# Kernel tuning notes

Hardware: AMD Instinct MI355X
Metric: run time of the kernel (lower is better)

## Reference

```python
import jax, jax.numpy as jnp
import numpy as np

CURV_BOUNDS = (-2.0, 2.0)
THRESH = 0.01   # |k| below this -> Euclidean branch
EPS = 1e-5

B, S, D = 4, 2048, 512


def setup_inputs() -> dict:
    key = jax.random.key(0)
    ks = jax.random.split(key, 8)
    x = jax.random.normal(ks[0], (B, S, D), jnp.float32)
    sc = 1.0 / np.sqrt(D)  # ~ nn.Linear default init scale
    Wq = jax.random.uniform(ks[1], (D, D), jnp.float32, -sc, sc)
    bq = jax.random.uniform(ks[2], (D,), jnp.float32, -sc, sc)
    Wk = jax.random.uniform(ks[3], (D, D), jnp.float32, -sc, sc)
    bk = jax.random.uniform(ks[4], (D,), jnp.float32, -sc, sc)
    Wv = jax.random.uniform(ks[5], (D, D), jnp.float32, -sc, sc)
    bv = jax.random.uniform(ks[6], (D,), jnp.float32, -sc, sc)
    curvature_raw = jnp.float32(0.5)   # init_curvature
    temperature = jnp.float32(1.0)
    mask = jnp.triu(jnp.ones((S, S), dtype=bool), 1)  # causal: True = masked out
    return {"x": x, "Wq": Wq, "bq": bq, "Wk": Wk, "bk": bk, "Wv": Wv,
            "bv": bv, "curvature_raw": curvature_raw,
            "temperature": temperature, "mask": mask}


def _curvature(raw):
    k_min, k_max = CURV_BOUNDS
    return k_min + (k_max - k_min) * (jnp.tanh(raw) + 1.0) / 2.0


def _project(u, k):
    # project_to_manifold: identity (euclid), Poincare-ball clip (k<0), sphere renorm (k>0)
    n = jnp.sqrt(jnp.sum(u * u, axis=-1, keepdims=True) + 1e-12)
    absk = jnp.abs(k)
    sk = jnp.sqrt(jnp.maximum(absk, EPS))
    max_norm = (1.0 - 1e-3) / sk                      # ball radius 1/sqrt(|k|)
    u_hyp = u * jnp.minimum(1.0, max_norm / n)
    u_sph = u / (n * sk)                              # sphere radius 1/sqrt(k)
    return jnp.where(absk < THRESH, u, jnp.where(k < 0, u_hyp, u_sph))


def reference(x, Wq, bq, Wk, bk, Wv, bv, curvature_raw, temperature, mask):
    k = _curvature(curvature_raw)
    q = x @ Wq.T + bq
    kk = x @ Wk.T + bk
    v = x @ Wv.T + bv
    qm = _project(q, k)
    km = _project(kk, k)

    # pairwise quantities without materializing [B,S,S,D]
    dots = jnp.einsum('bid,bjd->bij', qm, km)         # [B,S,S]
    qn2 = jnp.sum(qm * qm, axis=-1)                   # [B,S]
    kn2 = jnp.sum(km * km, axis=-1)                   # [B,S]
    diff2 = jnp.maximum(qn2[:, :, None] + kn2[:, None, :] - 2.0 * dots, 0.0)

    absk = jnp.abs(k)
    sk = jnp.sqrt(jnp.maximum(absk, EPS))

    d_euc = jnp.sqrt(diff2 + 1e-12)
    # hyperbolic (Poincare ball, c=|k|): acosh(1 + 2c|x-y|^2 / ((1-c|x|^2)(1-c|y|^2))) / sqrt(c)
    denom = jnp.maximum((1.0 - absk * qn2)[:, :, None] * (1.0 - absk * kn2)[:, None, :], EPS)
    arg = 1.0 + 2.0 * absk * diff2 / denom
    d_hyp = jnp.arccosh(jnp.maximum(arg, 1.0 + 1e-7)) / sk
    # spherical (radius 1/sqrt(k)): arccos(k * <x,y>) / sqrt(k)
    cosang = jnp.clip(absk * dots, -1.0 + 1e-7, 1.0 - 1e-7)
    d_sph = jnp.arccos(cosang) / sk

    dist = jnp.where(absk < THRESH, d_euc, jnp.where(k < 0, d_hyp, d_sph))

    scores = -dist / (temperature + 1e-8)
    scores = jnp.where(mask[None, :, :], -jnp.inf, scores)
    attention = jax.nn.softmax(scores, axis=-1)       # [B,S,S]
    output = jnp.einsum('bij,bjd->bid', attention, v) # [B,S,D]
    return output, attention
```

## Files before the change

kernel.cpp:

```cpp
#include <hip/hip_runtime.h>
#include <hip/hip_bf16.h>
#include <math.h>

typedef unsigned short u16;
typedef float float4e __attribute__((ext_vector_type(4)));
typedef short short8 __attribute__((ext_vector_type(8)));
typedef unsigned short ushort8 __attribute__((ext_vector_type(8)));
typedef unsigned short u16x4 __attribute__((ext_vector_type(4)));

#define SEQ 2048
#define DIM 512
#define NB  4

__device__ __forceinline__ float bf2f(u16 h) {
    return __uint_as_float(((unsigned)h) << 16);
}
__device__ __forceinline__ u16 f2bf(float f) {
    __hip_bfloat16 h = __float2bfloat16(f);
    return *reinterpret_cast<u16*>(&h);
}
__device__ __forceinline__ float curv_of(float raw) {
    return -2.0f + 2.0f * (tanhf(raw) + 1.0f);
}
__device__ __forceinline__ float fast_acos(float x) {
    float ax = fabsf(x);
    float r = sqrtf(fmaxf(1.f - ax, 0.f)) *
              (1.5707288f + ax * (-0.2121144f + ax * (0.0742610f - 0.0187293f * ax)));
    return (x < 0.f) ? (3.14159265f - r) : r;
}
__device__ __forceinline__ void gl_lds16(const u16* g, u16* lds) {
    __builtin_amdgcn_global_load_lds(
        (const __attribute__((address_space(1))) unsigned int*)g,
        (__attribute__((address_space(3))) unsigned int*)lds, 16, 0, 0);
}

__global__ __launch_bounds__(256, 4) void qkv_kernel(
    const float* __restrict__ xf,
    const float* __restrict__ Wq, const float* __restrict__ Wk, const float* __restrict__ Wv,
    const float* __restrict__ bq, const float* __restrict__ bk, const float* __restrict__ bv,
    u16* __restrict__ C, u16* __restrict__ vT)
{
    int bn = blockIdx.x, bm = blockIdx.y;

    __shared__ __align__(16) u16 As[64 * 64];
    __shared__ __align__(16) u16 Bs[64 * 64];

    int t = threadIdx.x, wave = t >> 6, lane = t & 63;
    int wr = wave >> 1, wc = wave & 1;
    int lrow = lane & 15, quad = lane >> 4;
    int srow = lane >> 3, sc = lane & 7;

    const float* Af = xf + (size_t)(bm * 64) * 512;
    const float* Wsel = (bn < 8) ? Wq : (bn < 16 ? Wk : Wv);
    const float* Bf = Wsel + (size_t)((bn & 7) * 64) * 512;

    float4e acc[2][2];
#pragma unroll
    for (int i = 0; i < 2; i++)
#pragma unroll
        for (int j = 0; j < 2; j++) acc[i][j] = (float4e){0.f, 0.f, 0.f, 0.f};

    for (int kt = 0; kt < 8; ++kt) {
        int k0 = kt << 6;
        __syncthreads();
#pragma unroll
        for (int h = 0; h < 2; ++h) {
            int q = wave * 2 + h;
            int row = q * 8 + srow;
            int c = sc ^ srow;
            const float* ga = Af + (size_t)row * 512 + k0 + c * 8;
            float4 a0 = *(const float4*)ga, a1 = *(const float4*)(ga + 4);
            const float* gb = Bf + (size_t)row * 512 + k0 + c * 8;
            float4 b0 = *(const float4*)gb, b1 = *(const float4*)(gb + 4);
            ushort8 ha, hb;
            ha[0] = f2bf(a0.x); ha[1] = f2bf(a0.y); ha[2] = f2bf(a0.z); ha[3] = f2bf(a0.w);
            ha[4] = f2bf(a1.x); ha[5] = f2bf(a1.y); ha[6] = f2bf(a1.z); ha[7] = f2bf(a1.w);
            hb[0] = f2bf(b0.x); hb[1] = f2bf(b0.y); hb[2] = f2bf(b0.z); hb[3] = f2bf(b0.w);
            hb[4] = f2bf(b1.x); hb[5] = f2bf(b1.y); hb[6] = f2bf(b1.z); hb[7] = f2bf(b1.w);
            *(ushort8*)&As[(size_t)row * 64 + sc * 8] = ha;
            *(ushort8*)&Bs[(size_t)row * 64 + sc * 8] = hb;
        }
        __syncthreads();
#pragma unroll
        for (int s = 0; s < 2; ++s) {
            short8 af[2], bfr[2];
#pragma unroll
            for (int im = 0; im < 2; im++) {
                int R = wr * 32 + im * 16 + lrow;
                af[im] = *(const short8*)&As[R * 64 + (((s * 4 + quad) ^ (R & 7)) * 8)];
            }
#pragma unroll
            for (int in = 0; in < 2; in++) {
                int R = wc * 32 + in * 16 + lrow;
                bfr[in] = *(const short8*)&Bs[R * 64 + (((s * 4 + quad) ^ (R & 7)) * 8)];
            }
#pragma unroll
            for (int im = 0; im < 2; im++)
#pragma unroll
                for (int in = 0; in < 2; in++)
                    acc[im][in] = __builtin_amdgcn_mfma_f32_16x16x32_bf16(af[im], bfr[in], acc[im][in], 0, 0, 0);
        }
    }

#pragma unroll
    for (int im = 0; im < 2; im++)
#pragma unroll
        for (int in = 0; in < 2; in++) {
            int gi0 = bm * 64 + wr * 32 + im * 16 + quad * 4;
            int gj = bn * 64 + wc * 32 + in * 16 + lrow;
            float bias = (gj < 512) ? bq[gj] : (gj < 1024 ? bk[gj - 512] : bv[gj - 1024]);
            u16x4 pack;
#pragma unroll
            for (int r = 0; r < 4; r++) {
                u16 hv = f2bf(acc[im][in][r] + bias);
                C[(size_t)(gi0 + r) * 1536 + gj] = hv;
                pack[r] = hv;
            }
            if (gj >= 1024) {
                int bb = gi0 >> 11, s = gi0 & 2047;
                *(u16x4*)&vT[((size_t)bb * DIM + (gj - 1024)) * SEQ + s] = pack;
            }
        }
}

template<int MODE>
__global__ __launch_bounds__(256, 8) void gemm64_kernel(
    const u16* __restrict__ A, int lda, long long sA,
    const u16* __restrict__ Bt, int ldb, long long sB,
    void* __restrict__ Cv, int ldc, long long sC,
    float* __restrict__ lsum,
    const float* __restrict__ qn2v, const float* __restrict__ kn2v,
    const float* __restrict__ curvp, const float* __restrict__ tempp)
{
    int bn = blockIdx.x, b = blockIdx.z;
    int bm = (MODE == 2) ? (gridDim.y - 1 - blockIdx.y) : blockIdx.y;
    if (MODE == 1 && bn > bm) return;

    __shared__ __align__(16) u16 As[64 * 64];
    __shared__ __align__(16) u16 Bs[64 * 64];

    int t = threadIdx.x, wave = t >> 6, lane = t & 63;
    int wr = wave >> 1, wc = wave & 1;
    int lrow = lane & 15, quad = lane >> 4;
    int srow = lane >> 3, sc = lane & 7;

    const u16* Ab = A + (size_t)b * sA + (size_t)(bm * 64) * lda;
    const u16* Bb = Bt + (size_t)b * sB + (size_t)(bn * 64) * ldb;

    float4e acc[2][2];
#pragma unroll
    for (int i = 0; i < 2; i++)
#pragma unroll
        for (int j = 0; j < 2; j++) acc[i][j] = (float4e){0.f, 0.f, 0.f, 0.f};

    int kIters = (MODE == 2) ? (bm + 1) : 8;

    for (int kt = 0; kt < kIters; ++kt) {
        int k0 = kt << 6;
        __syncthreads();
#pragma unroll
        for (int h = 0; h < 2; ++h) {
            int q = wave * 2 + h;
            int row = q * 8 + srow;
            int c = sc ^ srow;
            gl_lds16(Ab + (size_t)row * lda + k0 + c * 8, &As[q * 512]);
            gl_lds16(Bb + (size_t)row * ldb + k0 + c * 8, &Bs[q * 512]);
        }
        __syncthreads();
#pragma unroll
        for (int s = 0; s < 2; ++s) {
            short8 af[2], bfr[2];
#pragma unroll
            for (int im = 0; im < 2; im++) {
                int R = wr * 32 + im * 16 + lrow;
                af[im] = *(const short8*)&As[R * 64 + (((s * 4 + quad) ^ (R & 7)) * 8)];
            }
#pragma unroll
            for (int in = 0; in < 2; in++) {
                int R = wc * 32 + in * 16 + lrow;
                bfr[in] = *(const short8*)&Bs[R * 64 + (((s * 4 + quad) ^ (R & 7)) * 8)];
            }
#pragma unroll
            for (int im = 0; im < 2; im++)
#pragma unroll
                for (int in = 0; in < 2; in++)
                    acc[im][in] = __builtin_amdgcn_mfma_f32_16x16x32_bf16(af[im], bfr[in], acc[im][in], 0, 0, 0);
        }
    }

    if (MODE == 1) {
        float kv = curv_of(curvp[0]);
        float absk = fabsf(kv);
        float sk = sqrtf(fmaxf(absk, 1e-5f));
        float invsk = 1.0f / sk;
        float invT = 1.0f / (tempp[0] + 1e-8f);
        u16* Cb = (u16*)Cv + (size_t)b * sC;

        float psum[2][4];
#pragma unroll
        for (int im = 0; im < 2; im++)
#pragma unroll
            for (int r = 0; r < 4; r++) psum[im][r] = 0.f;

#pragma unroll
        for (int im = 0; im < 2; im++) {
#pragma unroll
            for (int r = 0; r < 4; r++) {
                int gi = bm * 64 + wr * 32 + im * 16 + quad * 4 + r;
                float qn = qn2v[b * SEQ + gi];
#pragma unroll
                for (int in = 0; in < 2; in++) {
                    int gj = bn * 64 + wc * 32 + in * 16 + lrow;
                    float kn = kn2v[b * SEQ + gj];
                    float dot = acc[im][in][r];
                    float diff2 = fmaxf(qn + kn - 2.f * dot, 0.f);
                    float dist;
                    if (absk < 0.01f) {
                        dist = sqrtf(diff2 + 1e-12f);
                    } else if (kv < 0.f) {
                        float denom = fmaxf((1.f - absk * qn) * (1.f - absk * kn), 1e-5f);
                        float arg = fmaxf(1.f + 2.f * absk * diff2 / denom, 1.f + 1e-7f);
                        dist = acoshf(arg) * invsk;
                    } else {
                        float c = fminf(fmaxf(absk * dot, -1.f + 1e-7f), 1.f - 1e-7f);
                        dist = fast_acos(c) * invsk;
                    }
                    float s = -dist * invT;
                    float e = (gj <= gi) ? __expf(s) : 0.f;
                    Cb[(size_t)gi * ldc + gj] = f2bf(e);
                    psum[im][r] += e;
                }
            }
        }
#pragma unroll
        for (int im = 0; im < 2; im++)
#pragma unroll
            for (int r = 0; r < 4; r++) {
                float v = psum[im][r];
                v += __shfl_xor(v, 1);
                v += __shfl_xor(v, 2);
                v += __shfl_xor(v, 4);
                v += __shfl_xor(v, 8);
                if (lrow == 0) {
                    int gi = bm * 64 + wr * 32 + im * 16 + quad * 4 + r;
                    atomicAdd(&lsum[b * SEQ + gi], v);
                }
            }
    } else {
        float* Cb = (float*)Cv + (size_t)b * sC;
#pragma unroll
        for (int im = 0; im < 2; im++)
#pragma unroll
            for (int r = 0; r < 4; r++) {
                int gi = bm * 64 + wr * 32 + im * 16 + quad * 4 + r;
                float invl = 1.0f / lsum[b * SEQ + gi];
#pragma unroll
                for (int in = 0; in < 2; in++) {
                    int gd = bn * 64 + wc * 32 + in * 16 + lrow;
                    Cb[(size_t)gi * ldc + gd] = acc[im][in][r] * invl;
                }
            }
    }
}

__global__ __launch_bounds__(256) void project_kernel(
    const u16* __restrict__ qkvh,
    u16* __restrict__ qm, u16* __restrict__ km,
    float* __restrict__ qn2, float* __restrict__ kn2,
    float* __restrict__ lsum,
    const float* __restrict__ curvp)
{
    if (threadIdx.x < 4) lsum[blockIdx.x * 4 + threadIdx.x] = 0.f;

    int wave = threadIdx.x >> 6, lane = threadIdx.x & 63;
    int r = blockIdx.x * 4 + wave;
    float kv = curv_of(curvp[0]);
    float absk = fabsf(kv);
    float sk = sqrtf(fmaxf(absk, 1e-5f));

    const u16* qrow = qkvh + (size_t)r * 1536;
    ushort8 qh = *(const ushort8*)&qrow[lane * 8];
    ushort8 kh = *(const ushort8*)&qrow[512 + lane * 8];

    float qv[8], kw[8];
    float sq = 0.f, s2 = 0.f;
#pragma unroll
    for (int e = 0; e < 8; e++) {
        qv[e] = bf2f(qh[e]); sq += qv[e] * qv[e];
        kw[e] = bf2f(kh[e]); s2 += kw[e] * kw[e];
    }
#pragma unroll
    for (int off = 1; off < 64; off <<= 1) {
        sq += __shfl_xor(sq, off);
        s2 += __shfl_xor(s2, off);
    }

    float sclq, sclk;
    {
        float nq = sqrtf(sq + 1e-12f);
        float nk = sqrtf(s2 + 1e-12f);
        if (absk < 0.01f) { sclq = 1.f; sclk = 1.f; }
        else if (kv < 0.f) {
            float mx = (1.0f - 1e-3f) / sk;
            sclq = fminf(1.f, mx / nq);
            sclk = fminf(1.f, mx / nk);
        } else {
            sclq = 1.f / (nq * sk);
            sclk = 1.f / (nk * sk);
        }
    }
    if (lane == 0) {
        qn2[r] = sq * sclq * sclq;
        kn2[r] = s2 * sclk * sclk;
    }
    ushort8 qo, ko;
#pragma unroll
    for (int e = 0; e < 8; e++) {
        qo[e] = f2bf(qv[e] * sclq);
        ko[e] = f2bf(kw[e] * sclk);
    }
    *(ushort8*)&qm[(size_t)r * 512 + lane * 8] = qo;
    *(ushort8*)&km[(size_t)r * 512 + lane * 8] = ko;
}

__global__ __launch_bounds__(256) void norm_attn_kernel(
    const u16* __restrict__ attnH, const float* __restrict__ lsum,
    float* __restrict__ attnF)
{
    int i = blockIdx.x, b = blockIdx.y, t = threadIdx.x;
    float inv = 1.0f / lsum[b * SEQ + i];
    const u16* rowh = attnH + ((size_t)b * SEQ + i) * SEQ;
    float* row = attnF + ((size_t)b * SEQ + i) * SEQ;
    int L = i + 1;
    int j0 = t * 8;
    float4 lo, hi;
    if (j0 + 8 <= L) {
        ushort8 h = *(const ushort8*)&rowh[j0];
        lo.x = bf2f(h[0]) * inv; lo.y = bf2f(h[1]) * inv;
        lo.z = bf2f(h[2]) * inv; lo.w = bf2f(h[3]) * inv;
        hi.x = bf2f(h[4]) * inv; hi.y = bf2f(h[5]) * inv;
        hi.z = bf2f(h[6]) * inv; hi.w = bf2f(h[7]) * inv;
    } else {
        float v[8];
#pragma unroll
        for (int e = 0; e < 8; e++)
            v[e] = (j0 + e < L) ? bf2f(rowh[j0 + e]) * inv : 0.f;
        lo = (float4){v[0], v[1], v[2], v[3]};
        hi = (float4){v[4], v[5], v[6], v[7]};
    }
    *(float4*)&row[j0] = lo;
    *(float4*)&row[j0 + 4] = hi;
}

extern "C" void kernel_launch(void* const* d_in, const int* in_sizes, int n_in,
                              void* d_out, int out_size, void* d_ws, size_t ws_size,
                              hipStream_t stream) {
    (void)in_sizes; (void)n_in; (void)out_size; (void)ws_size;

    const float* x    = (const float*)d_in[0];
    const float* Wq   = (const float*)d_in[1];
    const float* bq   = (const float*)d_in[2];
    const float* Wk   = (const float*)d_in[3];
    const float* bk   = (const float*)d_in[4];
    const float* Wv   = (const float*)d_in[5];
    const float* bv   = (const float*)d_in[6];
    const float* curv = (const float*)d_in[7];
    const float* temp = (const float*)d_in[8];

    float* out   = (float*)d_out;
    float* attnF = out + (size_t)NB * SEQ * DIM;

    char* ws = (char*)d_ws;
    u16*   qkvh  = (u16*)(ws + 0);
    u16*   qm    = (u16*)(ws + 33554432);
    u16*   km    = (u16*)(ws + 41943040);
    u16*   vT    = (u16*)(ws + 50331648);
    float* qn2   = (float*)(ws + 58720256);
    float* kn2   = (float*)(ws + 58753024);
    float* lsum  = (float*)(ws + 58785792);
    u16*   attnH = (u16*)(ws + 0);

    qkv_kernel<<<dim3(1536 / 64, 8192 / 64, 1), 256, 0, stream>>>(
        x, Wq, Wk, Wv, bq, bk, bv, qkvh, vT);

    project_kernel<<<NB * SEQ / 4, 256, 0, stream>>>(qkvh, qm, km, qn2, kn2, lsum, curv);

    gemm64_kernel<1><<<dim3(SEQ / 64, SEQ / 64, NB), 256, 0, stream>>>(
        qm, 512, (long long)SEQ * DIM, km, 512, (long long)SEQ * DIM,
        (void*)attnH, SEQ, (long long)SEQ * SEQ,
        lsum, qn2, kn2, curv, temp);

    gemm64_kernel<2><<<dim3(DIM / 64, SEQ / 64, NB), 256, 0, stream>>>(
        attnH, SEQ, (long long)SEQ * SEQ, vT, SEQ, (long long)DIM * SEQ,
        (void*)out, DIM, (long long)SEQ * DIM,
        lsum, nullptr, nullptr, nullptr, nullptr);

    norm_attn_kernel<<<dim3(SEQ, NB), 256, 0, stream>>>(attnH, lsum, attnF);
}
```

Measured before the change: 244.8 us.

## Fold manifold projection scales into QK^T epilogue instead of materializing projected Q/K

The projection kernel no longer writes scaled bf16 copies of Q and K. It only stores per-row scale factors and norms. The scores GEMM reads the raw Q/K from the QKV buffer with stride 1024 and multiplies each dot product by the row and column scales in its epilogue. The QKV kernel stops writing V into the row-major buffer (V goes only to vT) and its occupancy hint is raised. This removes a full write and reread of Q/K, but the dot is now computed from unscaled bf16 values and scaled afterwards, which changes rounding slightly.

```diff
diff --git a/kernel.cpp b/kernel.cpp
--- a/kernel.cpp
+++ b/kernel.cpp
@@ -34,11 +34,11 @@
         (__attribute__((address_space(3))) unsigned int*)lds, 16, 0, 0);
 }
 
-__global__ __launch_bounds__(256, 4) void qkv_kernel(
+__global__ __launch_bounds__(256, 8) void qkv_kernel(
     const float* __restrict__ xf,
     const float* __restrict__ Wq, const float* __restrict__ Wk, const float* __restrict__ Wv,
     const float* __restrict__ bq, const float* __restrict__ bk, const float* __restrict__ bv,
-    u16* __restrict__ C, u16* __restrict__ vT)
+    u16* __restrict__ qk, u16* __restrict__ vT)
 {
     int bn = blockIdx.x, bm = blockIdx.y;
 
@@ -109,14 +109,14 @@
             int gi0 = bm * 64 + wr * 32 + im * 16 + quad * 4;
             int gj = bn * 64 + wc * 32 + in * 16 + lrow;
             float bias = (gj < 512) ? bq[gj] : (gj < 1024 ? bk[gj - 512] : bv[gj - 1024]);
-            u16x4 pack;
-#pragma unroll
-            for (int r = 0; r < 4; r++) {
-                u16 hv = f2bf(acc[im][in][r] + bias);
-                C[(size_t)(gi0 + r) * 1536 + gj] = hv;
-                pack[r] = hv;
-            }
-            if (gj >= 1024) {
+            if (gj < 1024) {
+#pragma unroll
+                for (int r = 0; r < 4; r++)
+                    qk[(size_t)(gi0 + r) * 1024 + gj] = f2bf(acc[im][in][r] + bias);
+            } else {
+                u16x4 pack;
+#pragma unroll
+                for (int r = 0; r < 4; r++) pack[r] = f2bf(acc[im][in][r] + bias);
                 int bb = gi0 >> 11, s = gi0 & 2047;
                 *(u16x4*)&vT[((size_t)bb * DIM + (gj - 1024)) * SEQ + s] = pack;
             }
@@ -130,6 +130,7 @@
     void* __restrict__ Cv, int ldc, long long sC,
     float* __restrict__ lsum,
     const float* __restrict__ qn2v, const float* __restrict__ kn2v,
+    const float* __restrict__ sclqv, const float* __restrict__ sclkv,
     const float* __restrict__ curvp, const float* __restrict__ tempp)
 {
     int bn = blockIdx.x, b = blockIdx.z;
@@ -208,11 +209,12 @@
             for (int r = 0; r < 4; r++) {
                 int gi = bm * 64 + wr * 32 + im * 16 + quad * 4 + r;
                 float qn = qn2v[b * SEQ + gi];
+                float sq = sclqv[b * SEQ + gi];
 #pragma unroll
                 for (int in = 0; in < 2; in++) {
                     int gj = bn * 64 + wc * 32 + in * 16 + lrow;
                     float kn = kn2v[b * SEQ + gj];
-                    float dot = acc[im][in][r];
+                    float dot = acc[im][in][r] * sq * sclkv[b * SEQ + gj];
                     float diff2 = fmaxf(qn + kn - 2.f * dot, 0.f);
                     float dist;
                     if (absk < 0.01f) {
@@ -264,9 +266,9 @@
 }
 
 __global__ __launch_bounds__(256) void project_kernel(
-    const u16* __restrict__ qkvh,
-    u16* __restrict__ qm, u16* __restrict__ km,
+    const u16* __restrict__ qk,
     float* __restrict__ qn2, float* __restrict__ kn2,
+    float* __restrict__ sclqv, float* __restrict__ sclkv,
     float* __restrict__ lsum,
     const float* __restrict__ curvp)
 {
@@ -278,16 +280,15 @@
     float absk = fabsf(kv);
     float sk = sqrtf(fmaxf(absk, 1e-5f));
 
-    const u16* qrow = qkvh + (size_t)r * 1536;
-    ushort8 qh = *(const ushort8*)&qrow[lane * 8];
-    ushort8 kh = *(const ushort8*)&qrow[512 + lane * 8];
-
-    float qv[8], kw[8];
+    const u16* row = qk + (size_t)r * 1024;
+    ushort8 qh = *(const ushort8*)&row[lane * 8];
+    ushort8 kh = *(const ushort8*)&row[512 + lane * 8];
+
     float sq = 0.f, s2 = 0.f;
 #pragma unroll
     for (int e = 0; e < 8; e++) {
-        qv[e] = bf2f(qh[e]); sq += qv[e] * qv[e];
-        kw[e] = bf2f(kh[e]); s2 += kw[e] * kw[e];
+        float qv = bf2f(qh[e]); sq += qv * qv;
+        float kw = bf2f(kh[e]); s2 += kw * kw;
     }
 #pragma unroll
     for (int off = 1; off < 64; off <<= 1) {
@@ -295,10 +296,10 @@
         s2 += __shfl_xor(s2, off);
     }
 
-    float sclq, sclk;
-    {
+    if (lane == 0) {
         float nq = sqrtf(sq + 1e-12f);
         float nk = sqrtf(s2 + 1e-12f);
+        float sclq, sclk;
         if (absk < 0.01f) { sclq = 1.f; sclk = 1.f; }
         else if (kv < 0.f) {
             float mx = (1.0f - 1e-3f) / sk;
@@ -308,19 +309,11 @@
             sclq = 1.f / (nq * sk);
             sclk = 1.f / (nk * sk);
         }
-    }
-    if (lane == 0) {
         qn2[r] = sq * sclq * sclq;
         kn2[r] = s2 * sclk * sclk;
-    }
-    ushort8 qo, ko;
-#pragma unroll
-    for (int e = 0; e < 8; e++) {
-        qo[e] = f2bf(qv[e] * sclq);
-        ko[e] = f2bf(kw[e] * sclk);
-    }
-    *(ushort8*)&qm[(size_t)r * 512 + lane * 8] = qo;
-    *(ushort8*)&km[(size_t)r * 512 + lane * 8] = ko;
+        sclqv[r] = sclq;
+        sclkv[r] = sclk;
+    }
 }
 
 __global__ __launch_bounds__(256) void norm_attn_kernel(
@@ -371,29 +364,29 @@
     float* attnF = out + (size_t)NB * SEQ * DIM;
 
     char* ws = (char*)d_ws;
-    u16*   qkvh  = (u16*)(ws + 0);
-    u16*   qm    = (u16*)(ws + 33554432);
-    u16*   km    = (u16*)(ws + 41943040);
+    u16*   attnH = (u16*)(ws + 0);
+    u16*   qk    = (u16*)(ws + 33554432);
     u16*   vT    = (u16*)(ws + 50331648);
     float* qn2   = (float*)(ws + 58720256);
     float* kn2   = (float*)(ws + 58753024);
-    float* lsum  = (float*)(ws + 58785792);
-    u16*   attnH = (u16*)(ws + 0);
+    float* sclq  = (float*)(ws + 58785792);
+    float* sclk  = (float*)(ws + 58818560);
+    float* lsum  = (float*)(ws + 58851328);
 
     qkv_kernel<<<dim3(1536 / 64, 8192 / 64, 1), 256, 0, stream>>>(
-        x, Wq, Wk, Wv, bq, bk, bv, qkvh, vT);
-
-    project_kernel<<<NB * SEQ / 4, 256, 0, stream>>>(qkvh, qm, km, qn2, kn2, lsum, curv);
+        x, Wq, Wk, Wv, bq, bk, bv, qk, vT);
+
+    project_kernel<<<NB * SEQ / 4, 256, 0, stream>>>(qk, qn2, kn2, sclq, sclk, lsum, curv);
 
     gemm64_kernel<1><<<dim3(SEQ / 64, SEQ / 64, NB), 256, 0, stream>>>(
-        qm, 512, (long long)SEQ * DIM, km, 512, (long long)SEQ * DIM,
+        qk, 1024, (long long)SEQ * 1024, qk + 512, 1024, (long long)SEQ * 1024,
         (void*)attnH, SEQ, (long long)SEQ * SEQ,
-        lsum, qn2, kn2, curv, temp);
+        lsum, qn2, kn2, sclq, sclk, curv, temp);
 
     gemm64_kernel<2><<<dim3(DIM / 64, SEQ / 64, NB), 256, 0, stream>>>(
         attnH, SEQ, (long long)SEQ * SEQ, vT, SEQ, (long long)DIM * SEQ,
         (void*)out, DIM, (long long)SEQ * DIM,
-        lsum, nullptr, nullptr, nullptr, nullptr);
+        lsum, nullptr, nullptr, nullptr, nullptr, nullptr, nullptr);
 
     norm_attn_kernel<<<dim3(SEQ, NB), 256, 0, stream>>>(attnH, lsum, attnF);
 }
```

Result: no change. 247.1 us (+1.0%).
